# Kernel tuning notes

Measured on AMD Instinct MI355X. Metric: run time of the kernel, lower is better.

## Reference

```python
import jax, jax.numpy as jnp
import numpy as np

DIM = 128
HEADS = 4
DIM_HEAD = 32
HIDDEN = HEADS * DIM_HEAD  # 128
EPS = 1e-5


def setup_inputs() -> dict:
    key = jax.random.key(0)
    ks = jax.random.split(key, 5)
    x = jax.random.normal(ks[0], (32, DIM, 64, 64), dtype=jnp.float32)
    # 1x1 convs are channel matmuls
    Wqkv = jax.random.normal(ks[1], (HIDDEN * 3, DIM), dtype=jnp.float32) * (1.0 / np.sqrt(DIM))
    Wout = jax.random.normal(ks[2], (DIM, HIDDEN), dtype=jnp.float32) * (1.0 / np.sqrt(HIDDEN))
    bout = jnp.zeros((DIM,), dtype=jnp.float32)
    ln_w = jnp.ones((DIM,), dtype=jnp.float32)
    ln_b = jnp.zeros((DIM,), dtype=jnp.float32)
    return {"x": x, "Wqkv": Wqkv, "Wout": Wout, "bout": bout, "ln_w": ln_w, "ln_b": ln_b}


def reference(x, Wqkv, Wout, bout, ln_w, ln_b):
    b, c, h, w = x.shape
    n = h * w
    xf = x.reshape(b, c, n)  # b c n
    qkv = jnp.einsum('oc,bcn->bon', Wqkv, xf)  # b (3*hidden) n
    q, k, v = jnp.split(qkv, 3, axis=1)
    # b (h d) n -> b h d n
    q = q.reshape(b, HEADS, DIM_HEAD, n)
    k = k.reshape(b, HEADS, DIM_HEAD, n)
    v = v.reshape(b, HEADS, DIM_HEAD, n)
    q = jax.nn.softmax(q, axis=-2)  # over feature dim d
    k = jax.nn.softmax(k, axis=-1)  # over spatial dim n
    context = jnp.einsum('bhdn,bhen->bhde', k, v)
    out = jnp.einsum('bhde,bhdn->bhen', context, q)  # b h e n
    out = out.reshape(b, HIDDEN, n)
    out = jnp.einsum('oc,bcn->bon', Wout, out) + bout[None, :, None]
    out = out.reshape(b, DIM, h, w)
    # LayerNorm2d over channel dim, biased variance
    mean = jnp.mean(out, axis=1, keepdims=True)
    var = jnp.var(out, axis=1, keepdims=True)
    out = (out - mean) / jnp.sqrt(var + EPS) * ln_w[None, :, None, None] + ln_b[None, :, None, None]
    return out
```

## Files before the change

### kernel.cpp

```cpp
#include <hip/hip_runtime.h>
#include <stdint.h>


constexpr int B_   = 32;
constexpr int C_   = 128;
constexpr int N_   = 4096;
constexpr int O3_  = 384;
constexpr int NSUB = 8;
constexpr int TPB_ = 8;

using short8  = __attribute__((ext_vector_type(8))) short;
using short4v = __attribute__((ext_vector_type(4))) short;
using float4v = __attribute__((ext_vector_type(4))) float;

__device__ __forceinline__ unsigned short bf16_rne(float f) {
    union { float f; uint32_t u; } v; v.f = f;
    uint32_t u = v.u;
    u += 0x7FFFu + ((u >> 16) & 1u);
    return (unsigned short)(u >> 16);
}
__device__ __forceinline__ float bf2f(unsigned short h) {
    union { uint32_t u; float f; } v; v.u = ((uint32_t)h) << 16; return v.f;
}

constexpr size_t OFF_WQ   = 0;
constexpr size_t OFF_WO   = 98304;
constexpr size_t OFF_SP   = 131072;
constexpr size_t OFF_CTXP = 262144;
constexpr size_t OFF_CTXN = 4456448;
constexpr size_t OFF_WBIG = 4718592;
constexpr size_t OFF_QSM  = 5767168;

__global__ __launch_bounds__(256) void k0_prep(const float* __restrict__ Wqkv,
                                               const float* __restrict__ Wout,
                                               unsigned short* __restrict__ wq,
                                               unsigned short* __restrict__ wo) {
    int t = blockIdx.x * 256 + threadIdx.x;
    if (t < O3_ * C_) wq[t] = bf16_rne(Wqkv[t]);
    if (t < C_ * C_)  wo[t] = bf16_rne(Wout[t]);
}

__global__ __launch_bounds__(1024) void k1_qkv(const float* __restrict__ x,
                                               const unsigned short* __restrict__ wq,
                                               unsigned short* __restrict__ qsm,
                                               float* __restrict__ ctx_part,
                                               float* __restrict__ S_part) {
    __shared__ __align__(16) unsigned short xs0[64 * 136];
    __shared__ __align__(16) unsigned short xs1[64 * 136];
    __shared__ __align__(16) unsigned short ek[128 * 72];
    __shared__ __align__(16) unsigned short vsh[128 * 72];

    const int b    = blockIdx.y;
    const int tblk = blockIdx.x;
    const int tid  = threadIdx.x;

    const int lane = tid & 63;
    const int wv   = tid >> 6;
    const int l15  = lane & 15;
    const int quad = lane >> 4;

    const float4v zero = {0.f, 0.f, 0.f, 0.f};

    short8 wfa[8];
    if (wv < 12) {
        const unsigned short* wqp = wq + (wv * 32 + l15) * C_ + quad * 8;
        #pragma unroll
        for (int kk = 0; kk < 4; kk++) {
            wfa[kk]     = *(const short8*)(wqp + kk * 32);
            wfa[4 + kk] = *(const short8*)(wqp + 16 * C_ + kk * 32);
        }
    }

    const int sid = tid & 255;
    const int snl = sid & 63;
    const int scg = sid >> 6;
    const float* xbase = x + ((size_t)b * C_ + (size_t)scg * 32) * N_ + snl;
    float xv[32];
    auto load_x = [&](int s) {
        const float* xp = xbase + (tblk * NSUB + s) * 64;
        #pragma unroll
        for (int i = 0; i < 32; i++) xv[i] = xp[(size_t)i * N_];
    };
    auto store_x = [&](unsigned short* xs) {
        unsigned short* dst = &xs[snl * 136 + scg * 32];
        #pragma unroll
        for (int ii = 0; ii < 4; ii++) {
            short8 v8;
            #pragma unroll
            for (int j = 0; j < 8; j++) v8[j] = (short)bf16_rne(xv[ii * 8 + j]);
            *(short8*)(dst + ii * 8) = v8;
        }
    };

    if (wv >= 12) { load_x(0); store_x(xs0); }
    unsigned short* xs_cur = xs0;
    unsigned short* xs_nxt = xs1;

    float4v cacc = zero;
    float s_acc  = 0.f;
    const int ch  = wv >> 2;
    const int cdt = (wv >> 1) & 1;
    const int cet = wv & 1;

    for (int s = 0; s < NSUB; s++) {
        const int ns = (tblk * NSUB + s) * 64;
        __syncthreads();

        if (wv < 12) {
            #pragma unroll
            for (int ct = 0; ct < 4; ct++) {
                short8 bfx[4];
                #pragma unroll
                for (int kk = 0; kk < 4; kk++)
                    bfx[kk] = *(const short8*)&xs_cur[(ct * 16 + l15) * 136 + kk * 32 + quad * 8];
                float4v acc0 = zero, acc1 = zero;
                #pragma unroll
                for (int kk = 0; kk < 4; kk++) {
                    acc0 = __builtin_amdgcn_mfma_f32_16x16x32_bf16(wfa[kk],     bfx[kk], acc0, 0, 0, 0);
                    acc1 = __builtin_amdgcn_mfma_f32_16x16x32_bf16(wfa[4 + kk], bfx[kk], acc1, 0, 0, 0);
                }
                const int ncol = ct * 16 + l15;
                if (wv < 4) {
                    float e0[4], e1[4], z = 0.f;
                    #pragma unroll
                    for (int r = 0; r < 4; r++) {
                        e0[r] = __expf(acc0[r]); e1[r] = __expf(acc1[r]);
                        z += e0[r] + e1[r];
                    }
                    z += __shfl_xor(z, 16, 64);
                    z += __shfl_xor(z, 32, 64);
                    const float iz = 1.0f / z;
                    unsigned short* qp = qsm + ((size_t)b * N_ + ns + ncol) * C_ + wv * 32 + quad * 4;
                    short4v s0, s1;
                    #pragma unroll
                    for (int r = 0; r < 4; r++) {
                        s0[r] = (short)bf16_rne(e0[r] * iz);
                        s1[r] = (short)bf16_rne(e1[r] * iz);
                    }
                    *(short4v*)qp = s0;
                    *(short4v*)(qp + 16) = s1;
                } else if (wv < 8) {
                    const int row0 = (wv - 4) * 32 + quad * 4;
                    #pragma unroll
                    for (int r = 0; r < 4; r++) {
                        ek[(row0 + r) * 72 + ncol]      = bf16_rne(__expf(acc0[r]));
                        ek[(row0 + 16 + r) * 72 + ncol] = bf16_rne(__expf(acc1[r]));
                    }
                } else {
                    const int row0 = (wv - 8) * 32 + quad * 4;
                    #pragma unroll
                    for (int r = 0; r < 4; r++) {
                        vsh[(row0 + r) * 72 + ncol]      = bf16_rne(acc0[r]);
                        vsh[(row0 + 16 + r) * 72 + ncol] = bf16_rne(acc1[r]);
                    }
                }
            }
        } else {
            if (s + 1 < NSUB) { load_x(s + 1); store_x(xs_nxt); }
        }
        __syncthreads();

        {
            const unsigned short* ap = &ek[(ch * 32 + cdt * 16 + l15) * 72 + quad * 8];
            const unsigned short* bp = &vsh[(ch * 32 + cet * 16 + l15) * 72 + quad * 8];
            #pragma unroll
            for (int kk = 0; kk < 2; kk++) {
                short8 a  = *(const short8*)(ap + kk * 32);
                short8 bb = *(const short8*)(bp + kk * 32);
                cacc = __builtin_amdgcn_mfma_f32_16x16x32_bf16(a, bb, cacc, 0, 0, 0);
            }
        }
        {
            const unsigned short* ep = &ek[(tid >> 3) * 72 + (tid & 7) * 8];
            short8 e0 = *(const short8*)ep;
            float ss = 0.f;
            #pragma unroll
            for (int j = 0; j < 8; j++) ss += bf2f((unsigned short)e0[j]);
            s_acc += ss;
        }
        { unsigned short* t = xs_cur; xs_cur = xs_nxt; xs_nxt = t; }
    }

    {
        float* cp = ctx_part + ((size_t)(b * TPB_ + tblk) << 12)
                  + ((ch * 32 + cdt * 16 + quad * 4) * 32 + cet * 16 + l15);
        #pragma unroll
        for (int r = 0; r < 4; r++) cp[r * 32] = cacc[r];
    }
    {
        float ss = s_acc;
        ss += __shfl_xor(ss, 1, 64);
        ss += __shfl_xor(ss, 2, 64);
        ss += __shfl_xor(ss, 4, 64);
        if ((tid & 7) == 0)
            S_part[(size_t)(b * TPB_ + tblk) * 128 + (tid >> 3)] = ss;
    }
}

__global__ __launch_bounds__(256) void k2a_reduce(const float* __restrict__ ctx_part,
                                                  const float* __restrict__ S_part,
                                                  unsigned short* __restrict__ ctxn) {
    __shared__ float Sinv[16];
    const int b     = blockIdx.x >> 3;
    const int chunk = blockIdx.x & 7;
    const int tid   = threadIdx.x;
    if (tid < 16) {
        const int hd = chunk * 16 + tid;
        float s = 0.f;
        #pragma unroll
        for (int t = 0; t < TPB_; t++)
            s += S_part[(size_t)(b * TPB_ + t) * 128 + hd];
        Sinv[tid] = 1.0f / s;
    }
    __syncthreads();
    #pragma unroll
    for (int j = 0; j < 2; j++) {
        const int ei = chunk * 512 + j * 256 + tid;
        float v = 0.f;
        #pragma unroll
        for (int t = 0; t < TPB_; t++)
            v += ctx_part[((size_t)(b * TPB_ + t) << 12) + ei];
        ctxn[(size_t)b * 4096 + ei] = bf16_rne(v * Sinv[(ei >> 5) - chunk * 16]);
    }
}

__global__ __launch_bounds__(512) void k2b_fold(const unsigned short* __restrict__ ctxn,
                                                const unsigned short* __restrict__ wo,
                                                unsigned short* __restrict__ wbig) {
    const int b   = blockIdx.x;
    const int tid = threadIdx.x;
    const int lane = tid & 63, wv = tid >> 6, l15 = lane & 15, quad = lane >> 4;
    const float4v zero = {0.f, 0.f, 0.f, 0.f};

    short8 a4[4], b8[8];
    #pragma unroll
    for (int h = 0; h < 4; h++)
        a4[h] = *(const short8*)(wo + (wv * 16 + l15) * C_ + h * 32 + quad * 8);
    #pragma unroll
    for (int ht = 0; ht < 8; ht++)
        b8[ht] = *(const short8*)(ctxn + (size_t)b * 4096
                                  + ((ht >> 1) * 32 + (ht & 1) * 16 + l15) * 32 + quad * 8);

    unsigned short* wb = wbig + (size_t)b * (C_ * C_);
    #pragma unroll
    for (int ht = 0; ht < 8; ht++) {
        float4v c4 = __builtin_amdgcn_mfma_f32_16x16x32_bf16(a4[ht >> 1], b8[ht], zero, 0, 0, 0);
        const int c     = wv * 4 + (ht >> 1);
        const int quadp = (ht & 1) * 2 + (l15 >> 3);
        #pragma unroll
        for (int r = 0; r < 4; r++)
            wb[((c * 64 + quadp * 16 + quad * 4 + r) << 3) + (l15 & 7)] = bf16_rne(c4[r]);
    }
}

__global__ __launch_bounds__(512) void k3_out(const unsigned short* __restrict__ qsm,
                                              const unsigned short* __restrict__ wbig,
                                              const float* __restrict__ bout,
                                              const float* __restrict__ lnw,
                                              const float* __restrict__ lnb,
                                              float* __restrict__ out) {
    __shared__ __align__(16) unsigned short wls[16384];

    const int b   = blockIdx.y;
    const int n0  = blockIdx.x * 128;
    const int tid = threadIdx.x;

    const int lane = tid & 63, wv = tid >> 6, l15 = lane & 15, quad = lane >> 4;
    const int nl = wv * 16 + l15;
    const size_t n = (size_t)n0 + nl;

    const float4v zero = {0.f, 0.f, 0.f, 0.f};

    short8 st[4];
    {
        const short8* src = (const short8*)(wbig + (size_t)b * (C_ * C_));
        #pragma unroll
        for (int i = 0; i < 4; i++) st[i] = src[i * 512 + tid];
    }
    short8 bq[4];
    #pragma unroll
    for (int kk = 0; kk < 4; kk++)
        bq[kk] = *(const short8*)(qsm + ((size_t)b * N_ + n) * C_ + kk * 32 + quad * 8);
    #pragma unroll
    for (int i = 0; i < 4; i++)
        *(short8*)&wls[(i * 512 + tid) * 8] = st[i];
    __syncthreads();

    float4v acc[8];
    #pragma unroll
    for (int ot = 0; ot < 8; ot++) {
        float4v a = zero;
        #pragma unroll
        for (int kk = 0; kk < 4; kk++) {
            short8 w = *(const short8*)&wls[(((ot * 4 + kk) * 64 + lane)) * 8];
            a = __builtin_amdgcn_mfma_f32_16x16x32_bf16(w, bq[kk], a, 0, 0, 0);
        }
        acc[ot] = a;
    }

    float sum = 0.f, sq = 0.f;
    #pragma unroll
    for (int ot = 0; ot < 8; ot++) {
        #pragma unroll
        for (int r = 0; r < 4; r++) {
            const int o = ot * 16 + quad * 4 + r;
            const float y = acc[ot][r] + bout[o];
            acc[ot][r] = y;
            sum += y; sq += y * y;
        }
    }
    sum += __shfl_xor(sum, 16, 64);
    sum += __shfl_xor(sum, 32, 64);
    sq  += __shfl_xor(sq, 16, 64);
    sq  += __shfl_xor(sq, 32, 64);
    const float mean = sum * (1.0f / 128.0f);
    const float var  = sq * (1.0f / 128.0f) - mean * mean;
    const float rstd = rsqrtf(var + 1e-5f);

    #pragma unroll
    for (int ot = 0; ot < 8; ot++) {
        #pragma unroll
        for (int r = 0; r < 4; r++) {
            const int o = ot * 16 + quad * 4 + r;
            out[((size_t)b * C_ + o) * N_ + n] = (acc[ot][r] - mean) * rstd * lnw[o] + lnb[o];
        }
    }
}

extern "C" void kernel_launch(void* const* d_in, const int* in_sizes, int n_in,
                              void* d_out, int out_size, void* d_ws, size_t ws_size,
                              hipStream_t stream) {
    const float* x    = (const float*)d_in[0];
    const float* Wqkv = (const float*)d_in[1];
    const float* Wout = (const float*)d_in[2];
    const float* bout = (const float*)d_in[3];
    const float* lnw  = (const float*)d_in[4];
    const float* lnb  = (const float*)d_in[5];
    float* out = (float*)d_out;

    char* ws = (char*)d_ws;
    unsigned short* wq   = (unsigned short*)(ws + OFF_WQ);
    unsigned short* wo   = (unsigned short*)(ws + OFF_WO);
    float* S_part        = (float*)(ws + OFF_SP);
    float* ctx_part      = (float*)(ws + OFF_CTXP);
    unsigned short* ctxn = (unsigned short*)(ws + OFF_CTXN);
    unsigned short* wbig = (unsigned short*)(ws + OFF_WBIG);
    unsigned short* qsm  = (unsigned short*)(ws + OFF_QSM);

    k0_prep<<<192, 256, 0, stream>>>(Wqkv, Wout, wq, wo);
    k1_qkv<<<dim3(TPB_, B_), 1024, 0, stream>>>(x, wq, qsm, ctx_part, S_part);
    k2a_reduce<<<B_ * 8, 256, 0, stream>>>(ctx_part, S_part, ctxn);
    k2b_fold<<<B_, 512, 0, stream>>>(ctxn, wo, wbig);
    k3_out<<<dim3(N_ / 128, B_), 512, 0, stream>>>(qsm, wbig, bout, lnw, lnb, out);
}
```

Baseline: 159.9 us.

## Deepen x prefetch in qkv kernel and process two column tiles per output block

In the qkv kernel, the loader waves now issue the global load of x two sub-steps ahead and convert/store the previous one, so global latency overlaps a full compute step. In the output kernel, each block handles two 128-column tiles, reusing the per-batch folded weight loaded into LDS, prefetching the next q tile, and caching bias/LN params in shared memory. The risks are higher register pressure from the extra buffered values and fewer blocks (half the grid) for k3, which could reduce occupancy.

```diff
diff --git a/kernel.cpp b/kernel.cpp
--- a/kernel.cpp
+++ b/kernel.cpp
@@ -76,23 +76,31 @@
     const int scg = sid >> 6;
     const float* xbase = x + ((size_t)b * C_ + (size_t)scg * 32) * N_ + snl;
     float xv[32];
+    short8 c16[4];
     auto load_x = [&](int s) {
         const float* xp = xbase + (tblk * NSUB + s) * 64;
         #pragma unroll
         for (int i = 0; i < 32; i++) xv[i] = xp[(size_t)i * N_];
     };
-    auto store_x = [&](unsigned short* xs) {
-        unsigned short* dst = &xs[snl * 136 + scg * 32];
+    auto conv_x = [&]() {
         #pragma unroll
         for (int ii = 0; ii < 4; ii++) {
             short8 v8;
             #pragma unroll
             for (int j = 0; j < 8; j++) v8[j] = (short)bf16_rne(xv[ii * 8 + j]);
-            *(short8*)(dst + ii * 8) = v8;
+            c16[ii] = v8;
         }
     };
-
-    if (wv >= 12) { load_x(0); store_x(xs0); }
+    auto store_c = [&](unsigned short* xs) {
+        unsigned short* dst = &xs[snl * 136 + scg * 32];
+        #pragma unroll
+        for (int ii = 0; ii < 4; ii++) *(short8*)(dst + ii * 8) = c16[ii];
+    };
+
+    if (wv >= 12) {
+        load_x(0); conv_x(); store_c(xs0);
+        load_x(1);
+    }
     unsigned short* xs_cur = xs0;
     unsigned short* xs_nxt = xs1;
 
@@ -156,7 +164,8 @@
                 }
             }
         } else {
-            if (s + 1 < NSUB) { load_x(s + 1); store_x(xs_nxt); }
+            if (s + 1 < NSUB) { conv_x(); store_c(xs_nxt); }
+            if (s + 2 < NSUB) load_x(s + 2);
         }
         __syncthreads();
 
@@ -260,16 +269,17 @@
                                               const float* __restrict__ lnb,
                                               float* __restrict__ out) {
     __shared__ __align__(16) unsigned short wls[16384];
-
-    const int b   = blockIdx.y;
-    const int n0  = blockIdx.x * 128;
-    const int tid = threadIdx.x;
+    __shared__ float lnp[384];
+
+    const int b    = blockIdx.y;
+    const int tseg = blockIdx.x;
+    const int tid  = threadIdx.x;
 
     const int lane = tid & 63, wv = tid >> 6, l15 = lane & 15, quad = lane >> 4;
     const int nl = wv * 16 + l15;
-    const size_t n = (size_t)n0 + nl;
 
     const float4v zero = {0.f, 0.f, 0.f, 0.f};
+    const size_t n0base = (size_t)tseg * 256;
 
     short8 st[4];
     {
@@ -277,53 +287,73 @@
         #pragma unroll
         for (int i = 0; i < 4; i++) st[i] = src[i * 512 + tid];
     }
-    short8 bq[4];
-    #pragma unroll
-    for (int kk = 0; kk < 4; kk++)
-        bq[kk] = *(const short8*)(qsm + ((size_t)b * N_ + n) * C_ + kk * 32 + quad * 8);
+    if (tid < 128) {
+        lnp[tid]       = bout[tid];
+        lnp[128 + tid] = lnw[tid];
+        lnp[256 + tid] = lnb[tid];
+    }
+    short8 bq[4], bqn[4];
+    {
+        const unsigned short* qp = qsm + ((size_t)b * N_ + n0base + nl) * C_ + quad * 8;
+        #pragma unroll
+        for (int kk = 0; kk < 4; kk++) bq[kk] = *(const short8*)(qp + kk * 32);
+    }
     #pragma unroll
     for (int i = 0; i < 4; i++)
         *(short8*)&wls[(i * 512 + tid) * 8] = st[i];
     __syncthreads();
 
-    float4v acc[8];
-    #pragma unroll
-    for (int ot = 0; ot < 8; ot++) {
-        float4v a = zero;
-        #pragma unroll
-        for (int kk = 0; kk < 4; kk++) {
-            short8 w = *(const short8*)&wls[(((ot * 4 + kk) * 64 + lane)) * 8];
-            a = __builtin_amdgcn_mfma_f32_16x16x32_bf16(w, bq[kk], a, 0, 0, 0);
-        }
-        acc[ot] = a;
-    }
-
-    float sum = 0.f, sq = 0.f;
-    #pragma unroll
-    for (int ot = 0; ot < 8; ot++) {
-        #pragma unroll
-        for (int r = 0; r < 4; r++) {
-            const int o = ot * 16 + quad * 4 + r;
-            const float y = acc[ot][r] + bout[o];
-            acc[ot][r] = y;
-            sum += y; sq += y * y;
-        }
-    }
-    sum += __shfl_xor(sum, 16, 64);
-    sum += __shfl_xor(sum, 32, 64);
-    sq  += __shfl_xor(sq, 16, 64);
-    sq  += __shfl_xor(sq, 32, 64);
-    const float mean = sum * (1.0f / 128.0f);
-    const float var  = sq * (1.0f / 128.0f) - mean * mean;
-    const float rstd = rsqrtf(var + 1e-5f);
-
-    #pragma unroll
-    for (int ot = 0; ot < 8; ot++) {
-        #pragma unroll
-        for (int r = 0; r < 4; r++) {
-            const int o = ot * 16 + quad * 4 + r;
-            out[((size_t)b * C_ + o) * N_ + n] = (acc[ot][r] - mean) * rstd * lnw[o] + lnb[o];
-        }
+    #pragma unroll
+    for (int t = 0; t < 2; t++) {
+        const size_t n = n0base + t * 128 + nl;
+        if (t == 0) {
+            const unsigned short* qp = qsm + ((size_t)b * N_ + n0base + 128 + nl) * C_ + quad * 8;
+            #pragma unroll
+            for (int kk = 0; kk < 4; kk++) bqn[kk] = *(const short8*)(qp + kk * 32);
+        }
+
+        float4v acc[8];
+        #pragma unroll
+        for (int ot = 0; ot < 8; ot++) {
+            float4v a = zero;
+            #pragma unroll
+            for (int kk = 0; kk < 4; kk++) {
+                short8 w = *(const short8*)&wls[((ot * 4 + kk) * 64 + lane) * 8];
+                a = __builtin_amdgcn_mfma_f32_16x16x32_bf16(w, bq[kk], a, 0, 0, 0);
+            }
+            acc[ot] = a;
+        }
+
+        float sum = 0.f, sq = 0.f;
+        #pragma unroll
+        for (int ot = 0; ot < 8; ot++) {
+            #pragma unroll
+            for (int r = 0; r < 4; r++) {
+                const int o = ot * 16 + quad * 4 + r;
+                const float y = acc[ot][r] + lnp[o];
+                acc[ot][r] = y;
+                sum += y; sq += y * y;
+            }
+        }
+        sum += __shfl_xor(sum, 16, 64);
+        sum += __shfl_xor(sum, 32, 64);
+        sq  += __shfl_xor(sq, 16, 64);
+        sq  += __shfl_xor(sq, 32, 64);
+        const float mean = sum * (1.0f / 128.0f);
+        const float var  = sq * (1.0f / 128.0f) - mean * mean;
+        const float rstd = rsqrtf(var + 1e-5f);
+
+        #pragma unroll
+        for (int ot = 0; ot < 8; ot++) {
+            #pragma unroll
+            for (int r = 0; r < 4; r++) {
+                const int o = ot * 16 + quad * 4 + r;
+                out[((size_t)b * C_ + o) * N_ + n] = (acc[ot][r] - mean) * rstd * lnp[128 + o] + lnp[256 + o];
+            }
+        }
+
+        #pragma unroll
+        for (int kk = 0; kk < 4; kk++) bq[kk] = bqn[kk];
     }
 }
 
@@ -351,5 +381,5 @@
     k1_qkv<<<dim3(TPB_, B_), 1024, 0, stream>>>(x, wq, qsm, ctx_part, S_part);
     k2a_reduce<<<B_ * 8, 256, 0, stream>>>(ctx_part, S_part, ctxn);
     k2b_fold<<<B_, 512, 0, stream>>>(ctxn, wo, wbig);
-    k3_out<<<dim3(N_ / 128, B_), 512, 0, stream>>>(qsm, wbig, bout, lnw, lnb, out);
-}
+    k3_out<<<dim3(16, B_), 512, 0, stream>>>(qsm, wbig, bout, lnw, lnb, out);
+}
```

Measured after the change: 158.4 us. Within noise of the previous version (-1.0%).
